# Optimization experiments

Hardware: AMD Instinct MI355X
Metric: run time of the kernel (lower is better)

## Reference

```python
import jax, jax.numpy as jnp
import numpy as np
from jax import lax


def _lstm(x, W_ih, W_hh, b_ih, b_hh, return_seq):
    """PyTorch-compatible single-layer LSTM, batch_first, zero init state.
    W_ih: [4H, D], W_hh: [4H, H], gate order (i, f, g, o).
    Returns [B, T, H] if return_seq else final hidden [B, H]."""
    B, T, _ = x.shape
    H = W_hh.shape[1]
    # Precompute input contribution for all timesteps: [B, T, 4H]
    xg = jnp.einsum('btd,gd->btg', x, W_ih) + b_ih + b_hh
    h0 = jnp.zeros((B, H), x.dtype)
    c0 = jnp.zeros((B, H), x.dtype)

    def step(carry, xt):
        h, c = carry
        g = xt + h @ W_hh.T  # [B, 4H]
        i, f, gg, o = jnp.split(g, 4, axis=-1)
        i = jax.nn.sigmoid(i)
        f = jax.nn.sigmoid(f)
        gg = jnp.tanh(gg)
        o = jax.nn.sigmoid(o)
        c = f * c + i * gg
        h = o * jnp.tanh(c)
        return (h, c), (h if return_seq else None)

    (hT, _), ys = lax.scan(step, (h0, c0), jnp.swapaxes(xg, 0, 1))
    if return_seq:
        return jnp.swapaxes(ys, 0, 1)  # [B, T, H]
    return hT


def setup_inputs() -> dict:
    key = jax.random.key(0)
    ks = jax.random.split(key, 12)
    B, T, D = 2048, 512, 64
    H1, H2 = 16, 4
    s = 0.1
    return {
        'x': jax.random.normal(ks[0], (B, T, D), jnp.float32),
        'W_ih1': jax.random.normal(ks[1], (4 * H1, D), jnp.float32) * s,
        'W_hh1': jax.random.normal(ks[2], (4 * H1, H1), jnp.float32) * s,
        'b_ih1': jax.random.normal(ks[3], (4 * H1,), jnp.float32) * s,
        'b_hh1': jax.random.normal(ks[4], (4 * H1,), jnp.float32) * s,
        'W_ih2': jax.random.normal(ks[5], (4 * H2, H1), jnp.float32) * s,
        'W_hh2': jax.random.normal(ks[6], (4 * H2, H2), jnp.float32) * s,
        'b_ih2': jax.random.normal(ks[7], (4 * H2,), jnp.float32) * s,
        'b_hh2': jax.random.normal(ks[8], (4 * H2,), jnp.float32) * s,
        'W_fc': jax.random.normal(ks[9], (D, H2), jnp.float32) * s,
        'b_fc': jax.random.normal(ks[10], (D,), jnp.float32) * s,
    }


def reference(x, W_ih1, W_hh1, b_ih1, b_hh1, W_ih2, W_hh2, b_ih2, b_hh2, W_fc, b_fc):
    y = _lstm(x, W_ih1, W_hh1, b_ih1, b_hh1, return_seq=True)  # [B, T, H1]
    y = jax.nn.relu(y)
    # Only the last timestep of lstm2 is used -> return final hidden state.
    y_last = _lstm(y, W_ih2, W_hh2, b_ih2, b_hh2, return_seq=False)  # [B, H2]
    out = y_last @ W_fc.T + b_fc  # [B, D]
    return jax.nn.sigmoid(out)
```

## Files before the change

kernel.cpp:

```cpp
#include <hip/hip_runtime.h>
#include <hip/hip_bf16.h>

#define T_ALL 512
#define TB 16
#define NB (T_ALL / TB)
#define LOG2E 1.44269504088896f
#define XSTR 68

typedef __attribute__((ext_vector_type(8))) short bf16x8;
typedef __attribute__((ext_vector_type(4))) float f32x4;

#define DPPF(v, CTRL) __uint_as_float((unsigned)__builtin_amdgcn_update_dpp(0, (int)__float_as_uint(v), (CTRL), 0xF, 0xF, true))
#define SWZF(v, PAT)  __uint_as_float((unsigned)__builtin_amdgcn_ds_swizzle((int)__float_as_uint(v), (PAT)))
#define BPERM(a, v)   __uint_as_float((unsigned)__builtin_amdgcn_ds_bpermute((a), (int)__float_as_uint(v)))

__device__ __forceinline__ unsigned pack2fast(float a, float b) {
    const unsigned ua = __float_as_uint(a) + 0x8000u;
    const unsigned ub = __float_as_uint(b) + 0x8000u;
    return __builtin_amdgcn_perm(ub, ua, 0x07060302u);
}
__device__ __forceinline__ bf16x8 make_frag(float4 lo, float4 hi) {
    union { unsigned u[4]; bf16x8 v; } r;
    r.u[0] = pack2fast(lo.x, lo.y);
    r.u[1] = pack2fast(lo.z, lo.w);
    r.u[2] = pack2fast(hi.x, hi.y);
    r.u[3] = pack2fast(hi.z, hi.w);
    return r.v;
}
__device__ __forceinline__ float4 scale4(float4 v, float s) {
    return make_float4(v.x * s, v.y * s, v.z * s, v.w * s);
}
__device__ __forceinline__ float4 relu4(float4 v) {
    return make_float4(fmaxf(v.x, 0.f), fmaxf(v.y, 0.f), fmaxf(v.z, 0.f), fmaxf(v.w, 0.f));
}
__device__ __forceinline__ float2 pkfma(float2 a, float2 b, float2 c) {
    return make_float2(fmaf(a.x, b.x, c.x), fmaf(a.y, b.y, c.y));
}
__device__ __forceinline__ float2 pkmul(float2 a, float2 b) {
    return make_float2(a.x * b.x, a.y * b.y);
}
__device__ __forceinline__ float tanh_c(float c) {
    return fmaf(2.0f, __builtin_amdgcn_rcpf(
        1.0f + __builtin_amdgcn_exp2f(-2.0f * LOG2E * c)), -1.0f);
}
__device__ __forceinline__ float fsigm(float x) {
    return __builtin_amdgcn_rcpf(1.0f + __builtin_amdgcn_exp2f(-LOG2E * x));
}

__global__ __launch_bounds__(192, 6)
void lstm_fused_v11(const float* __restrict__ x,
        const float* __restrict__ Wih1, const float* __restrict__ Whh1,
        const float* __restrict__ bih1, const float* __restrict__ bhh1,
        const float* __restrict__ Wih2, const float* __restrict__ Whh2,
        const float* __restrict__ bih2, const float* __restrict__ bhh2,
        const float* __restrict__ Wfc,  const float* __restrict__ bfc,
        float* __restrict__ out)
{
    __shared__ __align__(16) float xgl[2][TB * XSTR];
    __shared__ __align__(16) float h1l[2][TB][16];
    __shared__ __align__(16) float xg2l[TB * 16];

    const int tid = threadIdx.x;
    const int wid = tid >> 6;
    const int lane = tid & 63;
    const size_t b = blockIdx.x;
    const int tl = lane & 15;
    const int kh = lane >> 4;

    if (wid == 0) {
        const int T1 = lane & 3;
        const int j1 = lane >> 2;
        const float aA1 = (T1 == 2) ? 2.0f : 1.0f, aB1 = (T1 == 2) ? -1.0f : 0.0f;
        const int gidx = T1 * 16 + j1;

        float2 wrA0, wrA1, wrB0, wrB1, wrC0, wrC1, wrD0, wrD1;
        {
            const float sA = (T1 == 2) ? 2.0f * LOG2E : LOG2E;
            const float sB = ((T1 ^ 2) == 2) ? 2.0f * LOG2E : LOG2E;
            const float sC = ((T1 ^ 1) == 2) ? 2.0f * LOG2E : LOG2E;
            const float sD = ((T1 ^ 3) == 2) ? 2.0f * LOG2E : LOG2E;
            const float4 wa  = scale4(*(const float4*)(Whh1 + ((T1    ) * 16 + j1) * 16 + 4 * T1), sA);
            const float4 wbv = scale4(*(const float4*)(Whh1 + ((T1 ^ 2) * 16 + j1) * 16 + 4 * T1), sB);
            const float4 wc  = scale4(*(const float4*)(Whh1 + ((T1 ^ 1) * 16 + j1) * 16 + 4 * T1), sC);
            const float4 wd  = scale4(*(const float4*)(Whh1 + ((T1 ^ 3) * 16 + j1) * 16 + 4 * T1), sD);
            wrA0 = make_float2(wa.x, wa.y);   wrA1 = make_float2(wa.z, wa.w);
            wrB0 = make_float2(wbv.x, wbv.y); wrB1 = make_float2(wbv.z, wbv.w);
            wrC0 = make_float2(wc.x, wc.y);   wrC1 = make_float2(wc.z, wc.w);
            wrD0 = make_float2(wd.x, wd.y);   wrD1 = make_float2(wd.z, wd.w);
        }
        if (T1 == 0) h1l[1][15][j1] = 0.f;
        float c1r = 0.f, h1r = 0.f;
        __syncthreads();

        for (int c = 0; c < NB; ++c) {
            const float* xrow = &xgl[c & 1][0];
            const int rg = c & 1;
            const float* hprev0 = &h1l[rg ^ 1][15][0];
#pragma unroll
            for (int tt = 0; tt < TB; ++tt) {
                const float* hp = (tt == 0) ? hprev0 : &h1l[rg][tt - 1][0];
                const float4 gq = *(const float4*)(hp + 4 * T1);
                const float2 g01 = make_float2(gq.x, gq.y);
                const float2 g23 = make_float2(gq.z, gq.w);
                float2 aA = pkmul(wrA0, g01); aA = pkfma(wrA1, g23, aA);
                float2 aB = pkmul(wrB0, g01); aB = pkfma(wrB1, g23, aB);
                float2 aC = pkmul(wrC0, g01); aC = pkfma(wrC1, g23, aC);
                float2 aD = pkmul(wrD0, g01); aD = pkfma(wrD1, g23, aD);
                const float sA = aA.x + aA.y, sB2 = aB.x + aB.y;
                const float sC = aC.x + aC.y, sD = aD.x + aD.y;
                const float u0 = sA + DPPF(sC, 0xB1);
                const float u1 = sB2 + DPPF(sD, 0xB1);
                const float pre = u0 + DPPF(u1, 0x4E) + xrow[tt * XSTR + gidx];
                const float s1 = __builtin_amdgcn_rcpf(1.0f + __builtin_amdgcn_exp2f(-pre));
                const float act = fmaf(aA1, s1, aB1);
                const float fv = DPPF(act, 0x55);
                const float gv = DPPF(act, 0xAA);
                const float ov = DPPF(act, 0xFF);
                c1r = fmaf(fv, c1r, act * gv);
                h1r = ov * tanh_c(c1r);
                if (T1 == 0) h1l[rg][tt][j1] = h1r;
            }
            __syncthreads();
        }
    } else if (wid == 1) {
        const int m2 = lane >> 4;
        const int T2 = (lane >> 2) & 3;
        const int s2 = lane & 3;
        const int row2 = T2 * 4 + m2;
        const float sc2 = (T2 == 2) ? 2.0f * LOG2E : LOG2E;
        const float aA2 = (T2 == 2) ? 2.0f : 1.0f, aB2 = (T2 == 2) ? -1.0f : 0.0f;
        const float w2h = Whh2[row2 * 4 + s2] * sc2;
        const int ahs = s2 << 6;

        bf16x8 wA2;
        {
            union { unsigned u[4]; bf16x8 v; } z;
            z.u[0] = z.u[1] = z.u[2] = z.u[3] = 0u;
            wA2 = z.v;
            if (kh < 2) {
                const float scr = ((tl >> 2) == 2) ? 2.0f * LOG2E : LOG2E;
                const float* wp = Wih2 + tl * 16 + kh * 8;
                wA2 = make_frag(scale4(*(const float4*)wp, scr),
                                scale4(*(const float4*)(wp + 4), scr));
            }
        }
        f32x4 bias2v;
#pragma unroll
        for (int r = 0; r < 4; ++r) {
            const int g = 4 * kh + r;
            bias2v[r] = (bih2[g] + bhh2[g]) * (((g >> 2) == 2) ? 2.0f * LOG2E : LOG2E);
        }
        const float4 wfc = *(const float4*)(Wfc + lane * 4);
        const float bfcv = bfc[lane];
        float c2r = 0.f, h2v = 0.f, h2s = 0.f;
        __syncthreads();

#define GATES2(RG) do { \
    bf16x8 _bf; \
    { union { unsigned u[4]; bf16x8 v; } _z; _z.u[0]=_z.u[1]=_z.u[2]=_z.u[3]=0u; _bf = _z.v; } \
    if (kh < 2) { \
        const float4 _h0 = *(const float4*)&h1l[RG][tl][8 * kh]; \
        const float4 _h1 = *(const float4*)&h1l[RG][tl][8 * kh + 4]; \
        _bf = make_frag(relu4(_h0), relu4(_h1)); \
    } \
    f32x4 _acc = bias2v; \
    _acc = __builtin_amdgcn_mfma_f32_16x16x32_bf16(wA2, _bf, _acc, 0, 0, 0); \
    _Pragma("unroll") \
    for (int _r = 0; _r < 4; ++_r) \
        xg2l[tl * 16 + 4 * kh + _r] = _acc[_r]; \
} while (0)

#define LSTM2_STEP(TT) do { \
    const float _xg2 = xg2l[(TT) * 16 + row2]; \
    float _p2 = w2h * h2s; \
    _p2 += DPPF(_p2, 0xB1); \
    _p2 += DPPF(_p2, 0x4E); \
    _p2 += _xg2; \
    const float _act2 = fmaf(aA2, \
        __builtin_amdgcn_rcpf(1.0f + __builtin_amdgcn_exp2f(-_p2)), aB2); \
    const float _fv2 = SWZF(_act2, 0x101F); \
    const float _gv2 = SWZF(_act2, 0x201F); \
    const float _ov2 = SWZF(_act2, 0x301F); \
    c2r = fmaf(_fv2, c2r, _act2 * _gv2);      \
    h2v = _ov2 * tanh_c(c2r); \
    h2s = BPERM(ahs, h2v); \
} while (0)

        for (int c = 0; c < NB; ++c) {
            if (c >= 1) {
                GATES2((c - 1) & 1);
#pragma unroll
                for (int tt = 0; tt < TB; ++tt)
                    LSTM2_STEP(tt);
            }
            __syncthreads();
        }
        GATES2((NB - 1) & 1);
#pragma unroll
        for (int tt = 0; tt < TB; ++tt)
            LSTM2_STEP(tt);

        const float hq0 = __shfl(h2v, 0);
        const float hq1 = __shfl(h2v, 16);
        const float hq2 = __shfl(h2v, 32);
        const float hq3 = __shfl(h2v, 48);
        float accf = bfcv;
        accf = fmaf(wfc.x, hq0, accf);
        accf = fmaf(wfc.y, hq1, accf);
        accf = fmaf(wfc.z, hq2, accf);
        accf = fmaf(wfc.w, hq3, accf);
        out[b * 64 + lane] = fsigm(accf);
#undef GATES2
#undef LSTM2_STEP
    } else {
        bf16x8 wb[4][2];
        float bias1[4];
#pragma unroll
        for (int n = 0; n < 4; ++n) {
            const float scn = (n == 2) ? 2.0f * LOG2E : LOG2E;
#pragma unroll
            for (int kk = 0; kk < 2; ++kk) {
                const float* wp = Wih1 + (size_t)(n * 16 + tl) * 64 + kk * 32 + kh * 8;
                wb[n][kk] = make_frag(scale4(*(const float4*)wp, scn),
                                      scale4(*(const float4*)(wp + 4), scn));
            }
            bias1[n] = (bih1[n * 16 + tl] + bhh1[n * 16 + tl]) * scn;
        }
        const float* xb = x + b * (size_t)(T_ALL * 64);
        float4 xpf[4];

#define LOADX(CH) do { \
    const float* _src = xb + (size_t)(CH) * (TB * 64); \
    _Pragma("unroll") \
    for (int _kk = 0; _kk < 2; ++_kk) \
        _Pragma("unroll") \
        for (int _hf = 0; _hf < 2; ++_hf) \
            xpf[_kk * 2 + _hf] = *(const float4*)(_src + tl * 64 + _kk * 32 + kh * 8 + _hf * 4); \
} while (0)

#define MFMA_XG(BUF) do { \
    bf16x8 _a0 = make_frag(xpf[0], xpf[1]); \
    bf16x8 _a1 = make_frag(xpf[2], xpf[3]); \
    _Pragma("unroll") \
    for (int _n = 0; _n < 4; ++_n) { \
        f32x4 _acc = {bias1[_n], bias1[_n], bias1[_n], bias1[_n]}; \
        _acc = __builtin_amdgcn_mfma_f32_16x16x32_bf16(_a0, wb[_n][0], _acc, 0, 0, 0); \
        _acc = __builtin_amdgcn_mfma_f32_16x16x32_bf16(_a1, wb[_n][1], _acc, 0, 0, 0); \
        _Pragma("unroll") \
        for (int _r = 0; _r < 4; ++_r) \
            xgl[BUF][(kh * 4 + _r) * XSTR + _n * 16 + tl] = _acc[_r]; \
    } \
} while (0)

        LOADX(0);
        MFMA_XG(0);
        LOADX(1);
        __syncthreads();

        for (int c = 0; c < NB; ++c) {
            if (c + 1 < NB) {
                bf16x8 a0s = make_frag(xpf[0], xpf[1]);
                bf16x8 a1s = make_frag(xpf[2], xpf[3]);
                if (c + 2 < NB) LOADX(c + 2);
#pragma unroll
                for (int n = 0; n < 4; ++n) {
                    f32x4 acc = {bias1[n], bias1[n], bias1[n], bias1[n]};
                    acc = __builtin_amdgcn_mfma_f32_16x16x32_bf16(a0s, wb[n][0], acc, 0, 0, 0);
                    acc = __builtin_amdgcn_mfma_f32_16x16x32_bf16(a1s, wb[n][1], acc, 0, 0, 0);
#pragma unroll
                    for (int r = 0; r < 4; ++r)
                        xgl[(c + 1) & 1][(kh * 4 + r) * XSTR + n * 16 + tl] = acc[r];
                }
            }
            __syncthreads();
        }
#undef LOADX
#undef MFMA_XG
    }
}

extern "C" void kernel_launch(void* const* d_in, const int* in_sizes, int n_in,
                              void* d_out, int out_size, void* d_ws, size_t ws_size,
                              hipStream_t stream) {
    const float* x    = (const float*)d_in[0];
    const float* Wih1 = (const float*)d_in[1];
    const float* Whh1 = (const float*)d_in[2];
    const float* bih1 = (const float*)d_in[3];
    const float* bhh1 = (const float*)d_in[4];
    const float* Wih2 = (const float*)d_in[5];
    const float* Whh2 = (const float*)d_in[6];
    const float* bih2 = (const float*)d_in[7];
    const float* bhh2 = (const float*)d_in[8];
    const float* Wfc  = (const float*)d_in[9];
    const float* bfc  = (const float*)d_in[10];
    float* out = (float*)d_out;

    lstm_fused_v11<<<dim3(2048), dim3(192), 0, stream>>>(
        x, Wih1, Whh1, bih1, bhh1, Wih2, Whh2, bih2, bhh2, Wfc, bfc, out);
}
```

Baseline: 140.1 us.

## Transpose xgate LDS layout and broadcast h1 via bpermute in recurrence

Result: slower. 148.2 us (+5.8%).

```diff
diff --git a/kernel.cpp b/kernel.cpp
--- a/kernel.cpp
+++ b/kernel.cpp
@@ -5,7 +5,7 @@
 #define TB 16
 #define NB (T_ALL / TB)
 #define LOG2E 1.44269504088896f
-#define XSTR 68
+#define TSTR 20
 
 typedef __attribute__((ext_vector_type(8))) short bf16x8;
 typedef __attribute__((ext_vector_type(4))) float f32x4;
@@ -48,7 +48,7 @@
 }
 
 __global__ __launch_bounds__(192, 6)
-void lstm_fused_v11(const float* __restrict__ x,
+void lstm_fused_v12(const float* __restrict__ x,
         const float* __restrict__ Wih1, const float* __restrict__ Whh1,
         const float* __restrict__ bih1, const float* __restrict__ bhh1,
         const float* __restrict__ Wih2, const float* __restrict__ Whh2,
@@ -56,7 +56,7 @@
         const float* __restrict__ Wfc,  const float* __restrict__ bfc,
         float* __restrict__ out)
 {
-    __shared__ __align__(16) float xgl[2][TB * XSTR];
+    __shared__ __align__(16) float xgt[2][64 * TSTR];
     __shared__ __align__(16) float h1l[2][TB][16];
     __shared__ __align__(16) float xg2l[TB * 16];
 
@@ -88,37 +88,49 @@
             wrC0 = make_float2(wc.x, wc.y);   wrC1 = make_float2(wc.z, wc.w);
             wrD0 = make_float2(wd.x, wd.y);   wrD1 = make_float2(wd.z, wd.w);
         }
-        if (T1 == 0) h1l[1][15][j1] = 0.f;
+        const int ag0 = (16 * T1 + 0)  << 2;
+        const int ag1 = (16 * T1 + 4)  << 2;
+        const int ag2 = (16 * T1 + 8)  << 2;
+        const int ag3 = (16 * T1 + 12) << 2;
+
         float c1r = 0.f, h1r = 0.f;
         __syncthreads();
 
         for (int c = 0; c < NB; ++c) {
-            const float* xrow = &xgl[c & 1][0];
+            const float* xrow = &xgt[c & 1][gidx * TSTR];
             const int rg = c & 1;
-            const float* hprev0 = &h1l[rg ^ 1][15][0];
-#pragma unroll
-            for (int tt = 0; tt < TB; ++tt) {
-                const float* hp = (tt == 0) ? hprev0 : &h1l[rg][tt - 1][0];
-                const float4 gq = *(const float4*)(hp + 4 * T1);
-                const float2 g01 = make_float2(gq.x, gq.y);
-                const float2 g23 = make_float2(gq.z, gq.w);
-                float2 aA = pkmul(wrA0, g01); aA = pkfma(wrA1, g23, aA);
-                float2 aB = pkmul(wrB0, g01); aB = pkfma(wrB1, g23, aB);
-                float2 aC = pkmul(wrC0, g01); aC = pkfma(wrC1, g23, aC);
-                float2 aD = pkmul(wrD0, g01); aD = pkfma(wrD1, g23, aD);
-                const float sA = aA.x + aA.y, sB2 = aB.x + aB.y;
-                const float sC = aC.x + aC.y, sD = aD.x + aD.y;
-                const float u0 = sA + DPPF(sC, 0xB1);
-                const float u1 = sB2 + DPPF(sD, 0xB1);
-                const float pre = u0 + DPPF(u1, 0x4E) + xrow[tt * XSTR + gidx];
-                const float s1 = __builtin_amdgcn_rcpf(1.0f + __builtin_amdgcn_exp2f(-pre));
-                const float act = fmaf(aA1, s1, aB1);
-                const float fv = DPPF(act, 0x55);
-                const float gv = DPPF(act, 0xAA);
-                const float ov = DPPF(act, 0xFF);
-                c1r = fmaf(fv, c1r, act * gv);
-                h1r = ov * tanh_c(c1r);
-                if (T1 == 0) h1l[rg][tt][j1] = h1r;
+#pragma unroll
+            for (int t4 = 0; t4 < 4; ++t4) {
+                const float4 xq = *(const float4*)(xrow + t4 * 4);
+#pragma unroll
+                for (int u = 0; u < 4; ++u) {
+                    const int tt = t4 * 4 + u;
+                    const float xu = (u == 0) ? xq.x : (u == 1) ? xq.y
+                                   : (u == 2) ? xq.z : xq.w;
+                    const float g0 = BPERM(ag0, h1r);
+                    const float g1 = BPERM(ag1, h1r);
+                    const float g2 = BPERM(ag2, h1r);
+                    const float g3 = BPERM(ag3, h1r);
+                    const float2 g01 = make_float2(g0, g1);
+                    const float2 g23 = make_float2(g2, g3);
+                    float2 aA = pkmul(wrA0, g01); aA = pkfma(wrA1, g23, aA);
+                    float2 aB = pkmul(wrB0, g01); aB = pkfma(wrB1, g23, aB);
+                    float2 aC = pkmul(wrC0, g01); aC = pkfma(wrC1, g23, aC);
+                    float2 aD = pkmul(wrD0, g01); aD = pkfma(wrD1, g23, aD);
+                    const float sA = aA.x + aA.y, sB2 = aB.x + aB.y;
+                    const float sC = aC.x + aC.y, sD = aD.x + aD.y;
+                    const float u0 = sA + DPPF(sC, 0xB1);
+                    const float u1 = sB2 + DPPF(sD, 0xB1);
+                    const float pre = u0 + DPPF(u1, 0x4E) + xu;
+                    const float s1 = __builtin_amdgcn_rcpf(1.0f + __builtin_amdgcn_exp2f(-pre));
+                    const float act = fmaf(aA1, s1, aB1);
+                    const float fv = DPPF(act, 0x55);
+                    const float gv = DPPF(act, 0xAA);
+                    const float ov = DPPF(act, 0xFF);
+                    c1r = fmaf(fv, c1r, act * gv);
+                    h1r = ov * tanh_c(c1r);
+                    if (T1 == 0) h1l[rg][tt][j1] = h1r;
+                }
             }
             __syncthreads();
         }
@@ -246,9 +258,7 @@
         f32x4 _acc = {bias1[_n], bias1[_n], bias1[_n], bias1[_n]}; \
         _acc = __builtin_amdgcn_mfma_f32_16x16x32_bf16(_a0, wb[_n][0], _acc, 0, 0, 0); \
         _acc = __builtin_amdgcn_mfma_f32_16x16x32_bf16(_a1, wb[_n][1], _acc, 0, 0, 0); \
-        _Pragma("unroll") \
-        for (int _r = 0; _r < 4; ++_r) \
-            xgl[BUF][(kh * 4 + _r) * XSTR + _n * 16 + tl] = _acc[_r]; \
+        *(f32x4*)&xgt[BUF][(_n * 16 + tl) * TSTR + 4 * kh] = _acc; \
     } \
 } while (0)
 
@@ -267,9 +277,7 @@
                     f32x4 acc = {bias1[n], bias1[n], bias1[n], bias1[n]};
                     acc = __builtin_amdgcn_mfma_f32_16x16x32_bf16(a0s, wb[n][0], acc, 0, 0, 0);
                     acc = __builtin_amdgcn_mfma_f32_16x16x32_bf16(a1s, wb[n][1], acc, 0, 0, 0);
-#pragma unroll
-                    for (int r = 0; r < 4; ++r)
-                        xgl[(c + 1) & 1][(kh * 4 + r) * XSTR + n * 16 + tl] = acc[r];
+                    *(f32x4*)&xgt[(c + 1) & 1][(n * 16 + tl) * TSTR + 4 * kh] = acc;
                 }
             }
             __syncthreads();
@@ -295,6 +303,6 @@
     const float* bfc  = (const float*)d_in[10];
     float* out = (float*)d_out;
 
-    lstm_fused_v11<<<dim3(2048), dim3(192), 0, stream>>>(
+    lstm_fused_v12<<<dim3(2048), dim3(192), 0, stream>>>(
         x, Wih1, Whh1, bih1, bhh1, Wih2, Whh2, bih2, bhh2, Wfc, bfc, out);
 }
```
